# Kernel tuning notes

Hardware: AMD Instinct MI355X
Metric: run time of the kernel (lower is better)

## Reference

```python
import jax, jax.numpy as jnp
import numpy as np

N_NODES = 100000   # n_users + n_items
N_LAYERS = 3
EMBED = 128
N_EDGES = 3_200_000


def setup_inputs() -> dict:
    key = jax.random.key(0)
    k1, k2, k3, k4, k5 = jax.random.split(key, 5)
    embedding = jax.random.normal(k1, (N_NODES, EMBED), dtype=jnp.float32) * 0.1  # normal_(std=0.1)
    edge_src = jax.random.randint(k2, (N_EDGES,), 0, N_NODES)
    edge_dst = jax.random.randint(k3, (N_EDGES,), 0, N_NODES)
    edge_w = jax.random.uniform(k4, (N_EDGES,), dtype=jnp.float32)  # normalized adj values
    users = jax.random.randint(k5, (1024,), 0, 50000)
    return {"embedding": embedding, "edge_w": edge_w, "edge_src": edge_src,
            "edge_dst": edge_dst, "users": users, "n_users": 50000}


def reference(embedding, edge_w, edge_src, edge_dst, users, n_users):
    # LightGCN propagation: rep_{l+1}[dst] = sum_{edges} w_e * rep_l[src]
    rep = embedding
    acc = embedding  # running sum over layers (layer-0 included)
    for _ in range(N_LAYERS):
        msg = rep[edge_src] * edge_w[:, None]                      # [E, D]
        rep = jax.ops.segment_sum(msg, edge_dst, num_segments=N_NODES)
        acc = acc + rep
    final_rep = acc / (N_LAYERS + 1)                               # mean over layers
    # predict(users): scores = users_r @ all_items_r.T
    users_r = final_rep[users]                                     # [B, D]
    items_r = final_rep[n_users:]                                  # [n_items, D]
    scores = users_r @ items_r.T                                   # [B, n_items]
    return scores
```

## Files before the change

### kernel.cpp

```cpp
#include <hip/hip_runtime.h>
#include <hip/hip_bf16.h>
#include <hip/hip_fp16.h>

typedef float f4 __attribute__((ext_vector_type(4)));
typedef unsigned int u32x2 __attribute__((ext_vector_type(2)));
typedef _Float16 h8 __attribute__((ext_vector_type(8)));

__device__ __forceinline__ __half2 bits2h2(unsigned u) {
    union { unsigned u; __half2 h; } c; c.u = u; return c.h;
}
__device__ __forceinline__ unsigned h22bits(__half2 h) {
    union { unsigned u; __half2 h; } c; c.h = h; return c.u;
}

#define N_NODES   100000
#define EMBED     128
#define N_USERS_T 50000
#define N_ITEMS   50000

#define BSH   8
#define NB    391
#define NBLK  256

__global__ __launch_bounds__(256) void part_hist(const int* __restrict__ dst,
                                                 int* __restrict__ blkhist,
                                                 int n, int epb) {
    __shared__ int h[NB];
    for (int j = threadIdx.x; j < NB; j += 256) h[j] = 0;
    __syncthreads();
    int b = blockIdx.x, s = b * epb, e = min(n, s + epb);
    for (int i = s + (int)threadIdx.x; i < e; i += 256)
        atomicAdd(&h[dst[i] >> BSH], 1);
    __syncthreads();
    for (int j = threadIdx.x; j < NB; j += 256) blkhist[b * NB + j] = h[j];
}

__global__ __launch_bounds__(256) void part_cursors(const int* __restrict__ blkhist,
                                                    int* __restrict__ cursors,
                                                    int* __restrict__ total) {
    int bu = blockIdx.x, t = threadIdx.x;
    int v = blkhist[t * NB + bu];
    int lane = t & 63, wid = t >> 6;
    int x = v;
    #pragma unroll
    for (int off = 1; off < 64; off <<= 1) {
        int y = __shfl_up(x, off, 64);
        if (lane >= off) x += y;
    }
    __shared__ int ws4[4];
    if (lane == 63) ws4[wid] = x;
    __syncthreads();
    int add = 0;
    for (int j = 0; j < wid; ++j) add += ws4[j];
    cursors[t * NB + bu] = add + x - v;
    if (t == 255) total[bu] = add + x;
}

__global__ void bucket_base_scan(const int* __restrict__ total,
                                 int* __restrict__ base) {
    if (threadIdx.x == 0) {
        int s = 0;
        for (int j = 0; j < NB; ++j) { base[j] = s; s += total[j]; }
        base[NB] = s;
    }
}

__global__ __launch_bounds__(256) void part_scatter(const int* __restrict__ src,
                                                    const int* __restrict__ dst,
                                                    const float* __restrict__ w,
                                                    const int* __restrict__ cursors,
                                                    const int* __restrict__ base,
                                                    int2* __restrict__ part,
                                                    int n, int epb) {
    __shared__ int cur[NB];
    int b = blockIdx.x;
    for (int j = threadIdx.x; j < NB; j += 256)
        cur[j] = base[j] + cursors[b * NB + j];
    __syncthreads();
    int s = b * epb, e = min(n, s + epb);
    for (int i = s + (int)threadIdx.x; i < e; i += 256) {
        int d = dst[i];
        int bu = d >> BSH;
        int p = atomicAdd(&cur[bu], 1);
        int2 pe;
        pe.x = src[i] | ((d & 255) << 17);
        pe.y = __float_as_int(w[i]);
        part[p] = pe;
    }
}

__global__ __launch_bounds__(512) void bucket_csr(const int2* __restrict__ part,
                                                  const int* __restrict__ base,
                                                  int* __restrict__ off_end,
                                                  unsigned* __restrict__ ep,
                                                  int n_nodes) {
    __shared__ int cnt[256], cur2[256], ws4[4];
    int bu = blockIdx.x, t = threadIdx.x;
    int b0 = base[bu], b1 = base[bu + 1];
    if (t < 256) cnt[t] = 0;
    __syncthreads();
    for (int i = b0 + t; i < b1; i += 512)
        atomicAdd(&cnt[(part[i].x >> 17) & 255], 1);
    __syncthreads();
    int lane = t & 63, wid = t >> 6;
    int v = 0, x = 0;
    if (t < 256) {
        v = cnt[t]; x = v;
        #pragma unroll
        for (int off = 1; off < 64; off <<= 1) {
            int y = __shfl_up(x, off, 64);
            if (lane >= off) x += y;
        }
        if (lane == 63) ws4[wid] = x;
    }
    __syncthreads();
    if (t < 256) {
        int add = 0;
        for (int j = 0; j < wid; ++j) add += ws4[j];
        int incl = add + x;
        int node = (bu << BSH) + t;
        if (node < n_nodes) off_end[node] = b0 + incl;
        cur2[t] = b0 + incl - v;
    }
    __syncthreads();
    for (int i = b0 + t; i < b1; i += 512) {
        int2 pe = part[i];
        int dloc = (pe.x >> 17) & 255;
        int p = atomicAdd(&cur2[dloc], 1);
        float wf = __int_as_float(pe.y);
        int wq = (int)(wf * 32768.f + 0.5f);
        wq = min(max(wq, 0), 32767);
        ep[p] = (unsigned)(pe.x & 0x1FFFF) | ((unsigned)wq << 17);
    }
}

__global__ __launch_bounds__(256) void f2h_kernel(const float* __restrict__ in,
                                                  __half* __restrict__ out, int n4) {
    int i = blockIdx.x * 256 + threadIdx.x;
    if (i < n4) {
        f4 v = ((const f4*)in)[i];
        u32x2 o;
        o.x = h22bits(__floats2half2_rn(v.x, v.y));
        o.y = h22bits(__floats2half2_rn(v.z, v.w));
        ((u32x2*)out)[i] = o;
    }
}

__global__ __launch_bounds__(256) void layer_kernel(
        const __half* __restrict__ rep_in, __half* __restrict__ rep_out,
        const int* __restrict__ off_end, const unsigned* __restrict__ ep,
        int n_nodes) {
    int node = blockIdx.x * 4 + (threadIdx.x >> 6);
    if (node >= n_nodes) return;
    int lane = threadIdx.x & 63;
    int half = lane >> 5;
    int l32  = lane & 31;
    int beg = (node == 0) ? 0 : off_end[node - 1];
    int end = off_end[node];
    f4 s = {0.f, 0.f, 0.f, 0.f};
    const u32x2* rp = (const u32x2*)rep_in;
    for (int chunk = beg; chunk < end; chunk += 64) {
        int idx = chunk + lane;
        unsigned ev = (idx < end) ? ep[idx] : 0u;
        int m = end - chunk; if (m > 64) m = 64;
        #pragma unroll 8
        for (int j = 0; j < m; j += 2) {
            unsigned v = __shfl(ev, j + half);
            int   sn = v & 0x1FFFF;
            float wt = (float)(v >> 17) * (1.f / 32768.f);
            u32x2 rv = rp[(size_t)sn * 32 + l32];
            float2 f0 = __half22float2(bits2h2(rv.x));
            float2 f1 = __half22float2(bits2h2(rv.y));
            s.x = fmaf(wt, f0.x, s.x);
            s.y = fmaf(wt, f0.y, s.y);
            s.z = fmaf(wt, f1.x, s.z);
            s.w = fmaf(wt, f1.y, s.w);
        }
    }
    s.x += __shfl_xor(s.x, 32);
    s.y += __shfl_xor(s.y, 32);
    s.z += __shfl_xor(s.z, 32);
    s.w += __shfl_xor(s.w, 32);
    if (half == 0) {
        u32x2 ov;
        ov.x = h22bits(__floats2half2_rn(s.x, s.y));
        ov.y = h22bits(__floats2half2_rn(s.z, s.w));
        ((u32x2*)rep_out)[(size_t)node * 32 + l32] = ov;
    }
}

__global__ __launch_bounds__(256) void gather_users(const int* __restrict__ users,
                                                    const float* __restrict__ emb,
                                                    const __half* __restrict__ r1,
                                                    const __half* __restrict__ r2,
                                                    const __half* __restrict__ r3,
                                                    _Float16* __restrict__ ur, int nu) {
    int idx = blockIdx.x * 256 + threadIdx.x;
    int u = idx >> 5;
    int q = idx & 31;
    if (u >= nu) return;
    size_t row = (size_t)users[u];
    f4 e = *(const f4*)(emb + row * EMBED + q * 4);
    size_t p = row * 32 + q;
    u32x2 a = ((const u32x2*)r1)[p];
    u32x2 b = ((const u32x2*)r2)[p];
    u32x2 c = ((const u32x2*)r3)[p];
    float2 a0 = __half22float2(bits2h2(a.x)), a1 = __half22float2(bits2h2(a.y));
    float2 b0 = __half22float2(bits2h2(b.x)), b1 = __half22float2(bits2h2(b.y));
    float2 c0 = __half22float2(bits2h2(c.x)), c1 = __half22float2(bits2h2(c.y));
    float v0 = (e.x + a0.x + b0.x + c0.x) * 0.25f;
    float v1 = (e.y + a0.y + b0.y + c0.y) * 0.25f;
    float v2 = (e.z + a1.x + b1.x + c1.x) * 0.25f;
    float v3 = (e.w + a1.y + b1.y + c1.y) * 0.25f;
    u32x2 o;
    o.x = h22bits(__floats2half2_rn(v0, v1));
    o.y = h22bits(__floats2half2_rn(v2, v3));
    *(u32x2*)(ur + (size_t)u * EMBED + q * 4) = o;
}

__global__ __launch_bounds__(256) void copy_items(const float* __restrict__ emb,
                                                  const __half* __restrict__ r1,
                                                  const __half* __restrict__ r2,
                                                  const __half* __restrict__ r3,
                                                  _Float16* __restrict__ ir, int ni) {
    int idx = blockIdx.x * 256 + threadIdx.x;
    int i = idx >> 5;
    int q = idx & 31;
    if (i >= ni) return;
    size_t row = (size_t)(N_USERS_T + i);
    f4 e = *(const f4*)(emb + row * EMBED + q * 4);
    size_t p = row * 32 + q;
    u32x2 a = ((const u32x2*)r1)[p];
    u32x2 b = ((const u32x2*)r2)[p];
    u32x2 c = ((const u32x2*)r3)[p];
    float2 a0 = __half22float2(bits2h2(a.x)), a1 = __half22float2(bits2h2(a.y));
    float2 b0 = __half22float2(bits2h2(b.x)), b1 = __half22float2(bits2h2(b.y));
    float2 c0 = __half22float2(bits2h2(c.x)), c1 = __half22float2(bits2h2(c.y));
    float v0 = (e.x + a0.x + b0.x + c0.x) * 0.25f;
    float v1 = (e.y + a0.y + b0.y + c0.y) * 0.25f;
    float v2 = (e.z + a1.x + b1.x + c1.x) * 0.25f;
    float v3 = (e.w + a1.y + b1.y + c1.y) * 0.25f;
    u32x2 o;
    o.x = h22bits(__floats2half2_rn(v0, v1));
    o.y = h22bits(__floats2half2_rn(v2, v3));
    *(u32x2*)(ir + (size_t)i * EMBED + q * 4) = o;
}

__global__ __launch_bounds__(256) void gemm_mfma(const _Float16* __restrict__ U,
                                                 const _Float16* __restrict__ I,
                                                 float* __restrict__ C,
                                                 int nu, int nI) {
    int wave = threadIdx.x >> 6;
    int lane = threadIdx.x & 63;
    int i0 = (blockIdx.x * 4 + wave) * 64;
    int u0 = blockIdx.y * 64;
    if (i0 >= nI) return;
    int l16 = lane & 15;
    int kg  = lane >> 4;
    f4 acc[4][4] = {};
    bool inb[4];
    #pragma unroll
    for (int nt = 0; nt < 4; ++nt) inb[nt] = (i0 + nt * 16 + l16) < nI;
    #pragma unroll
    for (int kk = 0; kk < 4; ++kk) {
        const int ko = kk * 32 + kg * 8;
        h8 a[4], b[4];
        #pragma unroll
        for (int mt = 0; mt < 4; ++mt)
            a[mt] = *(const h8*)(U + (size_t)(u0 + mt * 16 + l16) * EMBED + ko);
        #pragma unroll
        for (int nt = 0; nt < 4; ++nt) {
            h8 z = {};
            b[nt] = inb[nt] ? *(const h8*)(I + (size_t)(i0 + nt * 16 + l16) * EMBED + ko) : z;
        }
        #pragma unroll
        for (int mt = 0; mt < 4; ++mt)
            #pragma unroll
            for (int nt = 0; nt < 4; ++nt)
                acc[mt][nt] = __builtin_amdgcn_mfma_f32_16x16x32_f16(a[mt], b[nt], acc[mt][nt], 0, 0, 0);
    }
    #pragma unroll
    for (int mt = 0; mt < 4; ++mt) {
        #pragma unroll
        for (int r = 0; r < 4; ++r) {
            int row = u0 + mt * 16 + kg * 4 + r;
            if (row >= nu) continue;
            float* Cr = C + (size_t)row * nI;
            #pragma unroll
            for (int nt = 0; nt < 4; ++nt) {
                int col = i0 + nt * 16 + l16;
                if (col < nI)
                    __builtin_nontemporal_store(acc[mt][nt][r], Cr + col);
            }
        }
    }
}

extern "C" void kernel_launch(void* const* d_in, const int* in_sizes, int n_in,
                              void* d_out, int out_size, void* d_ws, size_t ws_size,
                              hipStream_t stream) {
    const float* emb   = (const float*)d_in[0];
    const float* ew    = (const float*)d_in[1];
    const int*   esrc  = (const int*)d_in[2];
    const int*   edst  = (const int*)d_in[3];
    const int*   users = (const int*)d_in[4];
    const int n_edges = in_sizes[1];
    const int n_nodes = in_sizes[0] / EMBED;
    const int nu      = in_sizes[4];

    char* ws = (char*)d_ws;
    int*      off_end = (int*)ws;
    int*      blkhist = (int*)(ws + 400128);
    int*      cursors = (int*)(ws + 800640);
    int*      total   = (int*)(ws + 1201152);
    int*      bbase   = (int*)(ws + 1202816);
    unsigned* epc     = (unsigned*)(ws + 1204480);
    _Float16* ur      = (_Float16*)(ws + 1204480 + 12800000);
    _Float16* ir      = (_Float16*)(ws + 1204480 + 12800000 + 262144);

    __half* emb_h   = (__half*)d_out;
    __half* rep1_h  = emb_h + (size_t)12800000;
    __half* rep2_h  = emb_h + (size_t)2 * 12800000;
    __half* rep3_h  = emb_h + (size_t)3 * 12800000;
    int2*   part_ep = (int2*)(emb_h + (size_t)4 * 12800000);
    float*  out     = (float*)d_out;

    const int epb = (n_edges + NBLK - 1) / NBLK;

    part_hist   <<<NBLK, 256, 0, stream>>>(edst, blkhist, n_edges, epb);
    part_cursors<<<NB,   256, 0, stream>>>(blkhist, cursors, total);
    bucket_base_scan<<<1, 64, 0, stream>>>(total, bbase);
    part_scatter<<<NBLK, 256, 0, stream>>>(esrc, edst, ew, cursors, bbase,
                                           part_ep, n_edges, epb);
    bucket_csr  <<<NB,   512, 0, stream>>>(part_ep, bbase, off_end, epc, n_nodes);

    int n4 = n_nodes * EMBED / 4;
    f2h_kernel<<<(n4 + 255) / 256, 256, 0, stream>>>(emb, emb_h, n4);

    const int lgrid = (n_nodes + 3) / 4;
    layer_kernel<<<lgrid, 256, 0, stream>>>(emb_h,  rep1_h, off_end, epc, n_nodes);
    layer_kernel<<<lgrid, 256, 0, stream>>>(rep1_h, rep2_h, off_end, epc, n_nodes);
    layer_kernel<<<lgrid, 256, 0, stream>>>(rep2_h, rep3_h, off_end, epc, n_nodes);

    gather_users<<<(nu * 32 + 255) / 256, 256, 0, stream>>>(users, emb, rep1_h, rep2_h, rep3_h, ur, nu);
    copy_items<<<(N_ITEMS * 32 + 255) / 256, 256, 0, stream>>>(emb, rep1_h, rep2_h, rep3_h, ir, N_ITEMS);

    dim3 ggrid((N_ITEMS + 255) / 256, (nu + 63) / 64);
    gemm_mfma<<<ggrid, 256, 0, stream>>>(ur, ir, out, nu, N_ITEMS);
}
```

Measured before the change: 538.0 us.

## Slice embeddings into feature-column planes so layer gathers stay cache-resident

Reorganizes the fp16 node representations into 8 slices of 16 features each, so each slice plane is about 3.2 MB. The layer kernel now processes one slice per block, with two lanes per node each loading 16 bytes per edge. The goal is to keep each slice's random gather working set inside the L2/LLC. Edge lists are now read by every node-pair per slice with nontemporal loads, which re-reads the CSR 8 times per layer, and each gather fetch is only 32 bytes per node.

```diff
diff --git a/kernel.cpp b/kernel.cpp
--- a/kernel.cpp
+++ b/kernel.cpp
@@ -4,6 +4,7 @@
 
 typedef float f4 __attribute__((ext_vector_type(4)));
 typedef unsigned int u32x2 __attribute__((ext_vector_type(2)));
+typedef unsigned int u32x4 __attribute__((ext_vector_type(4)));
 typedef _Float16 h8 __attribute__((ext_vector_type(8)));
 
 __device__ __forceinline__ __half2 bits2h2(unsigned u) {
@@ -134,112 +135,131 @@
     }
 }
 
-__global__ __launch_bounds__(256) void f2h_kernel(const float* __restrict__ in,
-                                                  __half* __restrict__ out, int n4) {
-    int i = blockIdx.x * 256 + threadIdx.x;
-    if (i < n4) {
-        f4 v = ((const f4*)in)[i];
-        u32x2 o;
-        o.x = h22bits(__floats2half2_rn(v.x, v.y));
-        o.y = h22bits(__floats2half2_rn(v.z, v.w));
-        ((u32x2*)out)[i] = o;
-    }
-}
-
-__global__ __launch_bounds__(256) void layer_kernel(
-        const __half* __restrict__ rep_in, __half* __restrict__ rep_out,
+__global__ __launch_bounds__(256) void f2h_slice(const float* __restrict__ in,
+                                                 __half* __restrict__ out,
+                                                 int n_nodes) {
+    int s = blockIdx.y;
+    int t = blockIdx.x * 256 + threadIdx.x;
+    if (t >= n_nodes * 4) return;
+    int node = t >> 2, wq = t & 3;
+    f4 v = *(const f4*)(in + (size_t)node * EMBED + s * 16 + wq * 4);
+    u32x2 o;
+    o.x = h22bits(__floats2half2_rn(v.x, v.y));
+    o.y = h22bits(__floats2half2_rn(v.z, v.w));
+    ((u32x2*)out)[((size_t)s * n_nodes + node) * 4 + wq] = o;
+}
+
+__global__ __launch_bounds__(256) void layer_slice(
+        const __half* __restrict__ rin, __half* __restrict__ rout,
         const int* __restrict__ off_end, const unsigned* __restrict__ ep,
         int n_nodes) {
-    int node = blockIdx.x * 4 + (threadIdx.x >> 6);
+    int s    = blockIdx.x & 7;
+    int nb   = blockIdx.x >> 3;
+    int lane = threadIdx.x & 63;
+    int node = nb * 128 + (threadIdx.x >> 6) * 32 + (lane >> 1);
     if (node >= n_nodes) return;
-    int lane = threadIdx.x & 63;
-    int half = lane >> 5;
-    int l32  = lane & 31;
+    int h = lane & 1;
     int beg = (node == 0) ? 0 : off_end[node - 1];
     int end = off_end[node];
-    f4 s = {0.f, 0.f, 0.f, 0.f};
-    const u32x2* rp = (const u32x2*)rep_in;
-    for (int chunk = beg; chunk < end; chunk += 64) {
-        int idx = chunk + lane;
-        unsigned ev = (idx < end) ? ep[idx] : 0u;
-        int m = end - chunk; if (m > 64) m = 64;
-        #pragma unroll 8
-        for (int j = 0; j < m; j += 2) {
-            unsigned v = __shfl(ev, j + half);
-            int   sn = v & 0x1FFFF;
-            float wt = (float)(v >> 17) * (1.f / 32768.f);
-            u32x2 rv = rp[(size_t)sn * 32 + l32];
-            float2 f0 = __half22float2(bits2h2(rv.x));
-            float2 f1 = __half22float2(bits2h2(rv.y));
-            s.x = fmaf(wt, f0.x, s.x);
-            s.y = fmaf(wt, f0.y, s.y);
-            s.z = fmaf(wt, f1.x, s.z);
-            s.w = fmaf(wt, f1.y, s.w);
-        }
-    }
-    s.x += __shfl_xor(s.x, 32);
-    s.y += __shfl_xor(s.y, 32);
-    s.z += __shfl_xor(s.z, 32);
-    s.w += __shfl_xor(s.w, 32);
-    if (half == 0) {
-        u32x2 ov;
-        ov.x = h22bits(__floats2half2_rn(s.x, s.y));
-        ov.y = h22bits(__floats2half2_rn(s.z, s.w));
-        ((u32x2*)rep_out)[(size_t)node * 32 + l32] = ov;
-    }
+    const u32x4* rp = (const u32x4*)(rin + (size_t)s * n_nodes * 16);
+    u32x4*       wp = (u32x4*)(rout + (size_t)s * n_nodes * 16);
+    f4 sa = {0.f, 0.f, 0.f, 0.f};
+    f4 sb = {0.f, 0.f, 0.f, 0.f};
+
+    auto acc1 = [&](unsigned v, u32x4 rv) {
+        float wt = (float)(v >> 17) * (1.f / 32768.f);
+        float2 f0 = __half22float2(bits2h2(rv.x));
+        float2 f1 = __half22float2(bits2h2(rv.y));
+        float2 f2 = __half22float2(bits2h2(rv.z));
+        float2 f3 = __half22float2(bits2h2(rv.w));
+        sa.x = fmaf(wt, f0.x, sa.x); sa.y = fmaf(wt, f0.y, sa.y);
+        sa.z = fmaf(wt, f1.x, sa.z); sa.w = fmaf(wt, f1.y, sa.w);
+        sb.x = fmaf(wt, f2.x, sb.x); sb.y = fmaf(wt, f2.y, sb.y);
+        sb.z = fmaf(wt, f3.x, sb.z); sb.w = fmaf(wt, f3.y, sb.w);
+    };
+
+    int e = beg;
+    for (; e + 4 <= end; e += 4) {
+        unsigned v0 = __builtin_nontemporal_load(ep + e);
+        unsigned v1 = __builtin_nontemporal_load(ep + e + 1);
+        unsigned v2 = __builtin_nontemporal_load(ep + e + 2);
+        unsigned v3 = __builtin_nontemporal_load(ep + e + 3);
+        u32x4 r0 = rp[(v0 & 0x1FFFF) * 2 + h];
+        u32x4 r1 = rp[(v1 & 0x1FFFF) * 2 + h];
+        u32x4 r2 = rp[(v2 & 0x1FFFF) * 2 + h];
+        u32x4 r3 = rp[(v3 & 0x1FFFF) * 2 + h];
+        acc1(v0, r0); acc1(v1, r1); acc1(v2, r2); acc1(v3, r3);
+    }
+    for (; e < end; ++e) {
+        unsigned v = __builtin_nontemporal_load(ep + e);
+        u32x4 r = rp[(v & 0x1FFFF) * 2 + h];
+        acc1(v, r);
+    }
+    u32x4 ov;
+    ov.x = h22bits(__floats2half2_rn(sa.x, sa.y));
+    ov.y = h22bits(__floats2half2_rn(sa.z, sa.w));
+    ov.z = h22bits(__floats2half2_rn(sb.x, sb.y));
+    ov.w = h22bits(__floats2half2_rn(sb.z, sb.w));
+    wp[(size_t)node * 2 + h] = ov;
 }
 
 __global__ __launch_bounds__(256) void gather_users(const int* __restrict__ users,
-                                                    const float* __restrict__ emb,
+                                                    const __half* __restrict__ embS,
                                                     const __half* __restrict__ r1,
                                                     const __half* __restrict__ r2,
                                                     const __half* __restrict__ r3,
-                                                    _Float16* __restrict__ ur, int nu) {
+                                                    _Float16* __restrict__ ur,
+                                                    int nu, int n_nodes) {
     int idx = blockIdx.x * 256 + threadIdx.x;
     int u = idx >> 5;
     int q = idx & 31;
     if (u >= nu) return;
     size_t row = (size_t)users[u];
-    f4 e = *(const f4*)(emb + row * EMBED + q * 4);
-    size_t p = row * 32 + q;
+    int sl = q >> 2, wq = q & 3;
+    size_t p = ((size_t)sl * n_nodes + row) * 4 + wq;
+    u32x2 e = ((const u32x2*)embS)[p];
     u32x2 a = ((const u32x2*)r1)[p];
     u32x2 b = ((const u32x2*)r2)[p];
     u32x2 c = ((const u32x2*)r3)[p];
+    float2 e0 = __half22float2(bits2h2(e.x)), e1 = __half22float2(bits2h2(e.y));
     float2 a0 = __half22float2(bits2h2(a.x)), a1 = __half22float2(bits2h2(a.y));
     float2 b0 = __half22float2(bits2h2(b.x)), b1 = __half22float2(bits2h2(b.y));
     float2 c0 = __half22float2(bits2h2(c.x)), c1 = __half22float2(bits2h2(c.y));
-    float v0 = (e.x + a0.x + b0.x + c0.x) * 0.25f;
-    float v1 = (e.y + a0.y + b0.y + c0.y) * 0.25f;
-    float v2 = (e.z + a1.x + b1.x + c1.x) * 0.25f;
-    float v3 = (e.w + a1.y + b1.y + c1.y) * 0.25f;
+    float v0 = (e0.x + a0.x + b0.x + c0.x) * 0.25f;
+    float v1 = (e0.y + a0.y + b0.y + c0.y) * 0.25f;
+    float v2 = (e1.x + a1.x + b1.x + c1.x) * 0.25f;
+    float v3 = (e1.y + a1.y + b1.y + c1.y) * 0.25f;
     u32x2 o;
     o.x = h22bits(__floats2half2_rn(v0, v1));
     o.y = h22bits(__floats2half2_rn(v2, v3));
     *(u32x2*)(ur + (size_t)u * EMBED + q * 4) = o;
 }
 
-__global__ __launch_bounds__(256) void copy_items(const float* __restrict__ emb,
+__global__ __launch_bounds__(256) void copy_items(const __half* __restrict__ embS,
                                                   const __half* __restrict__ r1,
                                                   const __half* __restrict__ r2,
                                                   const __half* __restrict__ r3,
-                                                  _Float16* __restrict__ ir, int ni) {
+                                                  _Float16* __restrict__ ir,
+                                                  int ni, int n_nodes) {
     int idx = blockIdx.x * 256 + threadIdx.x;
     int i = idx >> 5;
     int q = idx & 31;
     if (i >= ni) return;
     size_t row = (size_t)(N_USERS_T + i);
-    f4 e = *(const f4*)(emb + row * EMBED + q * 4);
-    size_t p = row * 32 + q;
+    int sl = q >> 2, wq = q & 3;
+    size_t p = ((size_t)sl * n_nodes + row) * 4 + wq;
+    u32x2 e = ((const u32x2*)embS)[p];
     u32x2 a = ((const u32x2*)r1)[p];
     u32x2 b = ((const u32x2*)r2)[p];
     u32x2 c = ((const u32x2*)r3)[p];
+    float2 e0 = __half22float2(bits2h2(e.x)), e1 = __half22float2(bits2h2(e.y));
     float2 a0 = __half22float2(bits2h2(a.x)), a1 = __half22float2(bits2h2(a.y));
     float2 b0 = __half22float2(bits2h2(b.x)), b1 = __half22float2(bits2h2(b.y));
     float2 c0 = __half22float2(bits2h2(c.x)), c1 = __half22float2(bits2h2(c.y));
-    float v0 = (e.x + a0.x + b0.x + c0.x) * 0.25f;
-    float v1 = (e.y + a0.y + b0.y + c0.y) * 0.25f;
-    float v2 = (e.z + a1.x + b1.x + c1.x) * 0.25f;
-    float v3 = (e.w + a1.y + b1.y + c1.y) * 0.25f;
+    float v0 = (e0.x + a0.x + b0.x + c0.x) * 0.25f;
+    float v1 = (e0.y + a0.y + b0.y + c0.y) * 0.25f;
+    float v2 = (e1.x + a1.x + b1.x + c1.x) * 0.25f;
+    float v3 = (e1.y + a1.y + b1.y + c1.y) * 0.25f;
     u32x2 o;
     o.x = h22bits(__floats2half2_rn(v0, v1));
     o.y = h22bits(__floats2half2_rn(v2, v3));
@@ -318,11 +338,11 @@
     _Float16* ur      = (_Float16*)(ws + 1204480 + 12800000);
     _Float16* ir      = (_Float16*)(ws + 1204480 + 12800000 + 262144);
 
-    __half* emb_h   = (__half*)d_out;
-    __half* rep1_h  = emb_h + (size_t)12800000;
-    __half* rep2_h  = emb_h + (size_t)2 * 12800000;
-    __half* rep3_h  = emb_h + (size_t)3 * 12800000;
-    int2*   part_ep = (int2*)(emb_h + (size_t)4 * 12800000);
+    __half* emb_s   = (__half*)d_out;
+    __half* rep1_s  = emb_s + (size_t)12800000;
+    __half* rep2_s  = emb_s + (size_t)2 * 12800000;
+    __half* rep3_s  = emb_s + (size_t)3 * 12800000;
+    int2*   part_ep = (int2*)(emb_s + (size_t)4 * 12800000);
     float*  out     = (float*)d_out;
 
     const int epb = (n_edges + NBLK - 1) / NBLK;
@@ -334,16 +354,16 @@
                                            part_ep, n_edges, epb);
     bucket_csr  <<<NB,   512, 0, stream>>>(part_ep, bbase, off_end, epc, n_nodes);
 
-    int n4 = n_nodes * EMBED / 4;
-    f2h_kernel<<<(n4 + 255) / 256, 256, 0, stream>>>(emb, emb_h, n4);
-
-    const int lgrid = (n_nodes + 3) / 4;
-    layer_kernel<<<lgrid, 256, 0, stream>>>(emb_h,  rep1_h, off_end, epc, n_nodes);
-    layer_kernel<<<lgrid, 256, 0, stream>>>(rep1_h, rep2_h, off_end, epc, n_nodes);
-    layer_kernel<<<lgrid, 256, 0, stream>>>(rep2_h, rep3_h, off_end, epc, n_nodes);
-
-    gather_users<<<(nu * 32 + 255) / 256, 256, 0, stream>>>(users, emb, rep1_h, rep2_h, rep3_h, ur, nu);
-    copy_items<<<(N_ITEMS * 32 + 255) / 256, 256, 0, stream>>>(emb, rep1_h, rep2_h, rep3_h, ir, N_ITEMS);
+    dim3 fg((n_nodes * 4 + 255) / 256, 8);
+    f2h_slice<<<fg, 256, 0, stream>>>(emb, emb_s, n_nodes);
+
+    const int nbs = (n_nodes + 127) / 128;
+    layer_slice<<<nbs * 8, 256, 0, stream>>>(emb_s,  rep1_s, off_end, epc, n_nodes);
+    layer_slice<<<nbs * 8, 256, 0, stream>>>(rep1_s, rep2_s, off_end, epc, n_nodes);
+    layer_slice<<<nbs * 8, 256, 0, stream>>>(rep2_s, rep3_s, off_end, epc, n_nodes);
+
+    gather_users<<<(nu * 32 + 255) / 256, 256, 0, stream>>>(users, emb_s, rep1_s, rep2_s, rep3_s, ur, nu, n_nodes);
+    copy_items<<<(N_ITEMS * 32 + 255) / 256, 256, 0, stream>>>(emb_s, rep1_s, rep2_s, rep3_s, ir, N_ITEMS, n_nodes);
 
     dim3 ggrid((N_ITEMS + 255) / 256, (nu + 63) / 64);
     gemm_mfma<<<ggrid, 256, 0, stream>>>(ur, ir, out, nu, N_ITEMS);
```

New measurement: 946.8 us. +76.0%, slower.
